# Optimization experiments

Hardware: AMD Instinct MI355X
Metric: run time of the kernel (lower is better)

The kernel has to match this reference:

```python
import jax, jax.numpy as jnp
import numpy as np

B, N, E = 8, 20000, 320000
D_IN, D, D_OUT = 1, 64, 1
EPS = 1e-5


def _layer_norm(z, gamma, beta):
    mu = z.mean(-1, keepdims=True)
    var = ((z - mu) ** 2).mean(-1, keepdims=True)
    return gamma * (z - mu) / jnp.sqrt(var + EPS) + beta


def _mp_layer(h, src, dst, Ws, Wm, bias, gamma, beta):
    # h: (B, N, D); src/dst: (E,)
    h_self = h @ Ws                          # (B, N, D)
    msg = h[:, src, :] @ Wm                  # (B, E, D) gather + GEMM
    h_agg = jnp.zeros_like(h).at[:, dst, :].add(msg)   # scatter-add over nodes
    deg = jnp.zeros((N,), h.dtype).at[dst].add(1.0)
    deg = jnp.maximum(deg, 1.0)
    h_agg = h_agg / deg[None, :, None]
    z = h + jax.nn.relu(h_self + h_agg + bias)  # dropout = identity (eval)
    return _layer_norm(z, gamma, beta)


def setup_inputs() -> dict:
    key = jax.random.key(0)
    ks = jax.random.split(key, 16)
    # weights stored (in, out); y = x @ W + b. Kaiming-normal-ish scale.
    def kaiming(k, fin, fout):
        return jax.random.normal(k, (fin, fout), jnp.float32) * np.sqrt(2.0 / fin)
    inp = {
        "x": jax.random.normal(ks[0], (B, N, D_IN), jnp.float32),
        "edge_index": jax.random.randint(ks[1], (2, E), 0, N),
        "W_in": kaiming(ks[2], D_IN, D), "b_in": jnp.zeros((D,), jnp.float32),
        "Ws1": kaiming(ks[3], D, D), "Wm1": kaiming(ks[4], D, D),
        "bias1": jnp.zeros((D,), jnp.float32),
        "g1": jnp.ones((D,), jnp.float32), "be1": jnp.zeros((D,), jnp.float32),
        "Ws2": kaiming(ks[5], D, D), "Wm2": kaiming(ks[6], D, D),
        "bias2": jnp.zeros((D,), jnp.float32),
        "g2": jnp.ones((D,), jnp.float32), "be2": jnp.zeros((D,), jnp.float32),
        "Wh1": kaiming(ks[7], 2 * D, D), "bh1": jnp.zeros((D,), jnp.float32),
        "Wh2": kaiming(ks[8], D, D_OUT), "bh2": jnp.zeros((D_OUT,), jnp.float32),
    }
    return inp


def reference(x, edge_index, W_in, b_in, Ws1, Wm1, bias1, g1, be1,
              Ws2, Wm2, bias2, g2, be2, Wh1, bh1, Wh2, bh2):
    src, dst = edge_index[0], edge_index[1]
    h = jax.nn.relu(x @ W_in + b_in)                       # (B, N, D)
    h = _mp_layer(h, src, dst, Ws1, Wm1, bias1, g1, be1)
    h = _mp_layer(h, src, dst, Ws2, Wm2, bias2, g2, be2)
    graph_emb = jnp.concatenate([h.mean(axis=1), h.max(axis=1)], axis=-1)  # (B, 2D)
    out = jax.nn.relu(graph_emb @ Wh1 + bh1) @ Wh2 + bh2   # (B, D_OUT)
    return out
```

## Files before the change

### kernel.cpp

```cpp
#include <hip/hip_runtime.h>

#define BB 8
#define NN 20000
#define EE 320000
#define DD 64
#define ROWS (BB*NN)
#define TILES (ROWS/16)
#define EPS 1e-5f
#define CH 64


typedef __attribute__((ext_vector_type(4))) float float4v;
typedef __attribute__((ext_vector_type(8))) _Float16 half8v;

__device__ __forceinline__ int bcasti(int v, int l) {
  return __builtin_amdgcn_readlane(v, l);
}

__global__ __launch_bounds__(256) void k_encoder(const float* __restrict__ x,
    const float* __restrict__ Win, const float* __restrict__ bin,
    _Float16* __restrict__ hH, int* __restrict__ cnt) {
  int idx = blockIdx.x * 256 + threadIdx.x;
  if (idx < NN) cnt[idx] = 0;
  int g = idx * 8;
  if (g < NN * 512) {
    int n = g >> 9;
    int b = (g >> 6) & 7;
    int d0 = g & 63;
    float xv = x[(size_t)b * NN + n];
    float4 w0 = *(const float4*)&Win[d0];
    float4 w1 = *(const float4*)&Win[d0 + 4];
    float4 b0 = *(const float4*)&bin[d0];
    float4 b1 = *(const float4*)&bin[d0 + 4];
    float o[8];
    o[0] = fmaf(xv, w0.x, b0.x); o[1] = fmaf(xv, w0.y, b0.y);
    o[2] = fmaf(xv, w0.z, b0.z); o[3] = fmaf(xv, w0.w, b0.w);
    o[4] = fmaf(xv, w1.x, b1.x); o[5] = fmaf(xv, w1.y, b1.y);
    o[6] = fmaf(xv, w1.z, b1.z); o[7] = fmaf(xv, w1.w, b1.w);
    half8v ho;
#pragma unroll
    for (int k = 0; k < 8; ++k) ho[k] = (_Float16)(o[k] > 0.f ? o[k] : 0.f);
    *(half8v*)&hH[g] = ho;
  }
}

__global__ __launch_bounds__(256) void k_deg(const int* __restrict__ dst,
                                             int* __restrict__ cnt) {
  int e = blockIdx.x * 256 + threadIdx.x;
  if (e < EE) atomicAdd(&cnt[dst[e]], 1);
}

__global__ __launch_bounds__(1024) void k_scan(const int* __restrict__ cnt,
                                               int* __restrict__ rowptr,
                                               int* __restrict__ cur) {
  __shared__ int part[1024];
  int t = threadIdx.x;
  const int PER = (NN + 1023) / 1024;
  int base = t * PER;
  int s = 0;
#pragma unroll
  for (int i = 0; i < PER; ++i) {
    int idx = base + i;
    s += (idx < NN) ? cnt[idx] : 0;
  }
  part[t] = s;
  __syncthreads();
  for (int off = 1; off < 1024; off <<= 1) {
    int v = (t >= off) ? part[t - off] : 0;
    __syncthreads();
    part[t] += v;
    __syncthreads();
  }
  int run = (t > 0) ? part[t - 1] : 0;
#pragma unroll
  for (int i = 0; i < PER; ++i) {
    int idx = base + i;
    if (idx <= NN) rowptr[idx] = run;
    if (idx < NN) cur[idx] = run;
    run += (idx < NN) ? cnt[idx] : 0;
  }
}

__global__ __launch_bounds__(256) void k_fill(const int* __restrict__ src,
    const int* __restrict__ dst, int* __restrict__ cur,
    int* __restrict__ nbr) {
  int e = blockIdx.x * 256 + threadIdx.x;
  if (e < EE) {
    int pos = atomicAdd(&cur[dst[e]], 1);
    nbr[pos] = src[e];
  }
}

__global__ __launch_bounds__(256) void k_agg(const _Float16* __restrict__ hH,
    const int* __restrict__ rowptr, const int* __restrict__ nbr,
    _Float16* __restrict__ aggH) {
  int wid = (blockIdx.x * 256 + threadIdx.x) >> 6;
  int lane = threadIdx.x & 63;
  if (wid >= NN) return;
  int n = wid;
  int s0 = rowptr[n], s1 = rowptr[n + 1];
  float acc[8];
#pragma unroll
  for (int k = 0; k < 8; ++k) acc[k] = 0.f;
  for (int base = s0; base < s1; base += 64) {
    int m = s1 - base;
    if (m > 64) m = 64;
    int idxv = (base + lane < s1) ? nbr[base + lane] : 0;
    int j = 0;
    for (; j + 8 <= m; j += 8) {
      half8v v[8];
#pragma unroll
      for (int i = 0; i < 8; ++i) {
        int s = bcasti(idxv, j + i);
        v[i] = *(const half8v*)(hH + (size_t)s * 512 + lane * 8);
      }
#pragma unroll
      for (int k = 0; k < 8; ++k) {
        float t0 = (float)v[0][k] + (float)v[1][k];
        float t1 = (float)v[2][k] + (float)v[3][k];
        float t2 = (float)v[4][k] + (float)v[5][k];
        float t3 = (float)v[6][k] + (float)v[7][k];
        acc[k] += (t0 + t1) + (t2 + t3);
      }
    }
    for (; j + 4 <= m; j += 4) {
      half8v v[4];
#pragma unroll
      for (int i = 0; i < 4; ++i) {
        int s = bcasti(idxv, j + i);
        v[i] = *(const half8v*)(hH + (size_t)s * 512 + lane * 8);
      }
#pragma unroll
      for (int k = 0; k < 8; ++k) {
        acc[k] += ((float)v[0][k] + (float)v[1][k]) +
                  ((float)v[2][k] + (float)v[3][k]);
      }
    }
    for (; j < m; ++j) {
      int s = bcasti(idxv, j);
      half8v v = *(const half8v*)(hH + (size_t)s * 512 + lane * 8);
#pragma unroll
      for (int k = 0; k < 8; ++k) acc[k] += (float)v[k];
    }
  }
  int deg = s1 - s0;
  float iv = 1.0f / (float)(deg > 1 ? deg : 1);
  half8v o;
#pragma unroll
  for (int k = 0; k < 8; ++k) o[k] = (_Float16)(acc[k] * iv);
  *(half8v*)(aggH + (size_t)n * 512 + lane * 8) = o;
}

__global__ __launch_bounds__(256) void k_node_mfma(
    const _Float16* __restrict__ hH, const _Float16* __restrict__ aggH,
    const float* __restrict__ Ws, const float* __restrict__ Wm,
    const float* __restrict__ bias, const float* __restrict__ g,
    const float* __restrict__ be, _Float16* __restrict__ outH,
    int nwaves_total) {
  __shared__ _Float16 ldsw[16384];
  int tid = threadIdx.x;
  int lane = tid & 63;
  int cidx = lane & 15;
  int grp = lane >> 4;

  for (int m = 0; m < 2; ++m) {
    const float* W = m ? Wm : Ws;
    for (int slot = tid; slot < 512; slot += 256) {
      int c = slot >> 8;
      int t = (slot >> 6) & 3;
      int l = slot & 63;
      int k0 = c * 32 + (l >> 4) * 8;
      int col = t * 16 + (l & 15);
      half8v ohi, olo;
#pragma unroll
      for (int i = 0; i < 8; ++i) {
        float w = W[(k0 + i) * DD + col];
        _Float16 hi = (_Float16)w;
        ohi[i] = hi;
        olo[i] = (_Float16)(w - (float)hi);
      }
      *(half8v*)&ldsw[(((m * 2 + 0) * 2 + c) * 4 + t) * 512 + l * 8] = ohi;
      *(half8v*)&ldsw[(((m * 2 + 1) * 2 + c) * 4 + t) * 512 + l * 8] = olo;
    }
  }
  __syncthreads();

  float bias_c[4], gam_c[4], bet_c[4];
#pragma unroll
  for (int t = 0; t < 4; ++t) {
    int c = t * 16 + cidx;
    bias_c[t] = bias[c];
    gam_c[t] = g[c];
    bet_c[t] = be[c];
  }

  int gwave = blockIdx.x * 4 + (tid >> 6);
  for (int tile = gwave; tile < TILES; tile += nwaves_total) {
    int r0 = tile * 16;
    const _Float16* hp = hH + (size_t)(r0 + cidx) * DD;
    const _Float16* ap = aggH + (size_t)(r0 + cidx) * DD;
    half8v ah[2], am[2];
    ah[0] = *(const half8v*)(hp + grp * 8);
    ah[1] = *(const half8v*)(hp + 32 + grp * 8);
    am[0] = *(const half8v*)(ap + grp * 8);
    am[1] = *(const half8v*)(ap + 32 + grp * 8);

    float4v acc[4];
#pragma unroll
    for (int t = 0; t < 4; ++t) acc[t] = (float4v){0.f, 0.f, 0.f, 0.f};
#pragma unroll
    for (int t = 0; t < 4; ++t) {
#pragma unroll
      for (int c = 0; c < 2; ++c) {
        const half8v bsh = *(const half8v*)&ldsw[((0 + c) * 4 + t) * 512 + lane * 8];
        const half8v bsl = *(const half8v*)&ldsw[((2 + c) * 4 + t) * 512 + lane * 8];
        const half8v bmh = *(const half8v*)&ldsw[((4 + c) * 4 + t) * 512 + lane * 8];
        const half8v bml = *(const half8v*)&ldsw[((6 + c) * 4 + t) * 512 + lane * 8];
        acc[t] = __builtin_amdgcn_mfma_f32_16x16x32_f16(ah[c], bsh, acc[t], 0, 0, 0);
        acc[t] = __builtin_amdgcn_mfma_f32_16x16x32_f16(ah[c], bsl, acc[t], 0, 0, 0);
        acc[t] = __builtin_amdgcn_mfma_f32_16x16x32_f16(am[c], bmh, acc[t], 0, 0, 0);
        acc[t] = __builtin_amdgcn_mfma_f32_16x16x32_f16(am[c], bml, acc[t], 0, 0, 0);
      }
    }
#pragma unroll
    for (int j = 0; j < 4; ++j) {
      int row = r0 + grp * 4 + j;
      const _Float16* hr = hH + (size_t)row * DD;
      float zz[4];
      float part = 0.f;
#pragma unroll
      for (int t = 0; t < 4; ++t) {
        float hv = (float)hr[t * 16 + cidx];
        float v = acc[t][j] + bias_c[t];
        v = v > 0.f ? v : 0.f;
        zz[t] = hv + v;
        part += zz[t];
      }
      part += __shfl_xor(part, 1);
      part += __shfl_xor(part, 2);
      part += __shfl_xor(part, 4);
      part += __shfl_xor(part, 8);
      float mu = part * (1.0f / 64.0f);
      float vs = 0.f;
#pragma unroll
      for (int t = 0; t < 4; ++t) {
        float d = zz[t] - mu;
        vs += d * d;
      }
      vs += __shfl_xor(vs, 1);
      vs += __shfl_xor(vs, 2);
      vs += __shfl_xor(vs, 4);
      vs += __shfl_xor(vs, 8);
      float inv = rsqrtf(vs * (1.0f / 64.0f) + EPS);
#pragma unroll
      for (int t = 0; t < 4; ++t) {
        float val = fmaf(gam_c[t] * (zz[t] - mu), inv, bet_c[t]);
        outH[(size_t)row * DD + t * 16 + cidx] = (_Float16)val;
      }
    }
  }
}

__global__ __launch_bounds__(256) void k_reduce(const _Float16* __restrict__ hH,
    float* __restrict__ psum, float* __restrict__ pmax) {
  int lane = threadIdx.x & 63;
  int w = threadIdx.x >> 6;
  int b = blockIdx.x / CH;
  int chunk = blockIdx.x % CH;
  const int csz = (NN + CH - 1) / CH;
  int n0 = chunk * csz;
  int n1 = n0 + csz;
  if (n1 > NN) n1 = NN;
  float s = 0.f, m = -INFINITY;
  for (int n = n0 + w; n < n1; n += 4) {
    float v = (float)hH[(size_t)n * 512 + b * 64 + lane];
    s += v;
    m = fmaxf(m, v);
  }
  __shared__ float ls[4][DD], lm[4][DD];
  ls[w][lane] = s;
  lm[w][lane] = m;
  __syncthreads();
  if (w == 0) {
    float ss = ls[0][lane] + ls[1][lane] + ls[2][lane] + ls[3][lane];
    float mm = fmaxf(fmaxf(lm[0][lane], lm[1][lane]),
                     fmaxf(lm[2][lane], lm[3][lane]));
    psum[((size_t)b * CH + chunk) * DD + lane] = ss;
    pmax[((size_t)b * CH + chunk) * DD + lane] = mm;
  }
}

__global__ __launch_bounds__(512) void k_final(const float* __restrict__ psum,
    const float* __restrict__ pmax, const float* __restrict__ Wh1,
    const float* __restrict__ bh1, const float* __restrict__ Wh2,
    const float* __restrict__ bh2, float* __restrict__ out) {
  __shared__ float emb[BB][2 * DD];
  __shared__ float hid[BB][DD];
  int t = threadIdx.x;
  int b = t >> 6, d = t & 63;
  float s = 0.f, m = -INFINITY;
  for (int c = 0; c < CH; ++c) {
    s += psum[((size_t)b * CH + c) * DD + d];
    m = fmaxf(m, pmax[((size_t)b * CH + c) * DD + d]);
  }
  emb[b][d] = s * (1.0f / (float)NN);
  emb[b][DD + d] = m;
  __syncthreads();
  float acc = bh1[d];
#pragma unroll
  for (int k = 0; k < 2 * DD; ++k) acc = fmaf(emb[b][k], Wh1[k * DD + d], acc);
  hid[b][d] = acc > 0.f ? acc : 0.f;
  __syncthreads();
  if (d == 0) {
    float o = bh2[0];
    for (int j = 0; j < DD; ++j) o = fmaf(hid[b][j], Wh2[j], o);
    out[b] = o;
  }
}

extern "C" void kernel_launch(void* const* d_in, const int* in_sizes, int n_in,
                              void* d_out, int out_size, void* d_ws, size_t ws_size,
                              hipStream_t stream) {
  const float* x    = (const float*)d_in[0];
  const int*   ei   = (const int*)d_in[1];
  const float* Win  = (const float*)d_in[2];
  const float* bin  = (const float*)d_in[3];
  const float* Ws1  = (const float*)d_in[4];
  const float* Wm1  = (const float*)d_in[5];
  const float* bias1= (const float*)d_in[6];
  const float* g1   = (const float*)d_in[7];
  const float* be1  = (const float*)d_in[8];
  const float* Ws2  = (const float*)d_in[9];
  const float* Wm2  = (const float*)d_in[10];
  const float* bias2= (const float*)d_in[11];
  const float* g2   = (const float*)d_in[12];
  const float* be2  = (const float*)d_in[13];
  const float* Wh1  = (const float*)d_in[14];
  const float* bh1  = (const float*)d_in[15];
  const float* Wh2  = (const float*)d_in[16];
  const float* bh2  = (const float*)d_in[17];
  float* out = (float*)d_out;

  const int* src = ei;
  const int* dst = ei + EE;

  char* ws = (char*)d_ws;
  size_t off = 0;
  auto carve = [&](size_t bytes) {
    void* p = ws + off;
    off = (off + bytes + 255) & ~(size_t)255;
    return p;
  };
  const size_t h16bytes = sizeof(_Float16) * (size_t)ROWS * DD;
  _Float16* hA     = (_Float16*)carve(h16bytes);
  _Float16* hB     = (_Float16*)carve(h16bytes);
  _Float16* aggH   = (_Float16*)carve(h16bytes);
  int*      cnt    = (int*)carve(sizeof(int) * NN);
  int*      cur    = (int*)carve(sizeof(int) * NN);
  int*      rowptr = (int*)carve(sizeof(int) * (NN + 1));
  int*      nbr    = (int*)carve(sizeof(int) * EE);
  float*    psum   = (float*)carve(sizeof(float) * (size_t)BB * CH * DD);
  float*    pmax   = (float*)carve(sizeof(float) * (size_t)BB * CH * DD);

  const int NODE_BLOCKS = 2048;
  const int NODE_WAVES = NODE_BLOCKS * 4;

  k_encoder<<<(NN * 512 / 8 + 255) / 256, 256, 0, stream>>>(x, Win, bin, hA, cnt);

  k_deg<<<(EE + 255) / 256, 256, 0, stream>>>(dst, cnt);
  k_scan<<<1, 1024, 0, stream>>>(cnt, rowptr, cur);
  k_fill<<<(EE + 255) / 256, 256, 0, stream>>>(src, dst, cur, nbr);

  k_agg<<<(NN + 3) / 4, 256, 0, stream>>>(hA, rowptr, nbr, aggH);
  k_node_mfma<<<NODE_BLOCKS, 256, 0, stream>>>(hA, aggH, Ws1, Wm1, bias1, g1,
                                               be1, hB, NODE_WAVES);

  k_agg<<<(NN + 3) / 4, 256, 0, stream>>>(hB, rowptr, nbr, aggH);
  k_node_mfma<<<NODE_BLOCKS, 256, 0, stream>>>(hB, aggH, Ws2, Wm2, bias2, g2,
                                               be2, hA, NODE_WAVES);

  k_reduce<<<BB * CH, 256, 0, stream>>>(hA, psum, pmax);
  k_final<<<1, 512, 0, stream>>>(psum, pmax, Wh1, bh1, Wh2, bh2, out);
}
```

Baseline: 248.3 us.

## Fuse neighbor aggregation into MFMA node update kernel via LDS staging

Merges the gather/mean aggregation kernel into the node-update MFMA kernel. Each wave aggregates two nodes (16 rows of the node-major layout), stages the result in LDS and feeds it straight to the MFMA, so the aggH buffer is never written to or read back from global memory. Weight hi/lo fp16 splitting moves to a separate prep kernel that runs once, and each block just copies the packed weights into LDS. The cost is more LDS per block, and aggregation load imbalance across waves may now stall the MFMA phase.

New measurement: 380.0 us. 1.53x slower.

```diff
diff --git a/kernel.cpp b/kernel.cpp
--- a/kernel.cpp
+++ b/kernel.cpp
@@ -5,7 +5,7 @@
 #define EE 320000
 #define DD 64
 #define ROWS (BB*NN)
-#define TILES (ROWS/16)
+#define TILES (NN/2)
 #define EPS 1e-5f
 #define CH 64
 
@@ -91,98 +91,49 @@
   }
 }
 
-__global__ __launch_bounds__(256) void k_agg(const _Float16* __restrict__ hH,
-    const int* __restrict__ rowptr, const int* __restrict__ nbr,
-    _Float16* __restrict__ aggH) {
-  int wid = (blockIdx.x * 256 + threadIdx.x) >> 6;
-  int lane = threadIdx.x & 63;
-  if (wid >= NN) return;
-  int n = wid;
-  int s0 = rowptr[n], s1 = rowptr[n + 1];
-  float acc[8];
-#pragma unroll
-  for (int k = 0; k < 8; ++k) acc[k] = 0.f;
-  for (int base = s0; base < s1; base += 64) {
-    int m = s1 - base;
-    if (m > 64) m = 64;
-    int idxv = (base + lane < s1) ? nbr[base + lane] : 0;
-    int j = 0;
-    for (; j + 8 <= m; j += 8) {
-      half8v v[8];
-#pragma unroll
-      for (int i = 0; i < 8; ++i) {
-        int s = bcasti(idxv, j + i);
-        v[i] = *(const half8v*)(hH + (size_t)s * 512 + lane * 8);
-      }
-#pragma unroll
-      for (int k = 0; k < 8; ++k) {
-        float t0 = (float)v[0][k] + (float)v[1][k];
-        float t1 = (float)v[2][k] + (float)v[3][k];
-        float t2 = (float)v[4][k] + (float)v[5][k];
-        float t3 = (float)v[6][k] + (float)v[7][k];
-        acc[k] += (t0 + t1) + (t2 + t3);
-      }
-    }
-    for (; j + 4 <= m; j += 4) {
-      half8v v[4];
-#pragma unroll
-      for (int i = 0; i < 4; ++i) {
-        int s = bcasti(idxv, j + i);
-        v[i] = *(const half8v*)(hH + (size_t)s * 512 + lane * 8);
-      }
-#pragma unroll
-      for (int k = 0; k < 8; ++k) {
-        acc[k] += ((float)v[0][k] + (float)v[1][k]) +
-                  ((float)v[2][k] + (float)v[3][k]);
-      }
-    }
-    for (; j < m; ++j) {
-      int s = bcasti(idxv, j);
-      half8v v = *(const half8v*)(hH + (size_t)s * 512 + lane * 8);
-#pragma unroll
-      for (int k = 0; k < 8; ++k) acc[k] += (float)v[k];
-    }
-  }
-  int deg = s1 - s0;
-  float iv = 1.0f / (float)(deg > 1 ? deg : 1);
-  half8v o;
-#pragma unroll
-  for (int k = 0; k < 8; ++k) o[k] = (_Float16)(acc[k] * iv);
-  *(half8v*)(aggH + (size_t)n * 512 + lane * 8) = o;
-}
-
-__global__ __launch_bounds__(256) void k_node_mfma(
-    const _Float16* __restrict__ hH, const _Float16* __restrict__ aggH,
-    const float* __restrict__ Ws, const float* __restrict__ Wm,
+__global__ __launch_bounds__(256) void k_prep(const float* __restrict__ Ws1,
+    const float* __restrict__ Wm1, const float* __restrict__ Ws2,
+    const float* __restrict__ Wm2, _Float16* __restrict__ o1,
+    _Float16* __restrict__ o2) {
+  int gid = blockIdx.x * 256 + threadIdx.x;
+  int layer = gid >> 10;
+  int slot = gid & 1023;
+  int m = slot >> 9;
+  int c = (slot >> 8) & 1;
+  int t = (slot >> 6) & 3;
+  int l = slot & 63;
+  const float* W = layer ? (m ? Wm2 : Ws2) : (m ? Wm1 : Ws1);
+  _Float16* out = layer ? o2 : o1;
+  int k0 = c * 32 + (l >> 4) * 8;
+  int col = t * 16 + (l & 15);
+  half8v ohi, olo;
+#pragma unroll
+  for (int i = 0; i < 8; ++i) {
+    float w = W[(k0 + i) * DD + col];
+    _Float16 hi = (_Float16)w;
+    ohi[i] = hi;
+    olo[i] = (_Float16)(w - (float)hi);
+  }
+  *(half8v*)&out[(((m * 2 + 0) * 2 + c) * 4 + t) * 512 + l * 8] = ohi;
+  *(half8v*)&out[(((m * 2 + 1) * 2 + c) * 4 + t) * 512 + l * 8] = olo;
+}
+
+__global__ __launch_bounds__(256, 4) void k_agg_node(
+    const _Float16* __restrict__ hH, const int* __restrict__ rowptr,
+    const int* __restrict__ nbr, const _Float16* __restrict__ Wsp,
     const float* __restrict__ bias, const float* __restrict__ g,
     const float* __restrict__ be, _Float16* __restrict__ outH,
     int nwaves_total) {
   __shared__ _Float16 ldsw[16384];
+  __shared__ _Float16 ldsa[4][1024];
   int tid = threadIdx.x;
   int lane = tid & 63;
+  int wv = tid >> 6;
   int cidx = lane & 15;
   int grp = lane >> 4;
 
-  for (int m = 0; m < 2; ++m) {
-    const float* W = m ? Wm : Ws;
-    for (int slot = tid; slot < 512; slot += 256) {
-      int c = slot >> 8;
-      int t = (slot >> 6) & 3;
-      int l = slot & 63;
-      int k0 = c * 32 + (l >> 4) * 8;
-      int col = t * 16 + (l & 15);
-      half8v ohi, olo;
-#pragma unroll
-      for (int i = 0; i < 8; ++i) {
-        float w = W[(k0 + i) * DD + col];
-        _Float16 hi = (_Float16)w;
-        ohi[i] = hi;
-        olo[i] = (_Float16)(w - (float)hi);
-      }
-      *(half8v*)&ldsw[(((m * 2 + 0) * 2 + c) * 4 + t) * 512 + l * 8] = ohi;
-      *(half8v*)&ldsw[(((m * 2 + 1) * 2 + c) * 4 + t) * 512 + l * 8] = olo;
-    }
-  }
+  for (int i = tid; i < 2048; i += 256)
+    *(half8v*)&ldsw[i * 8] = *(const half8v*)&Wsp[i * 8];
   __syncthreads();
 
   float bias_c[4], gam_c[4], bet_c[4];
@@ -194,16 +145,71 @@
     bet_c[t] = be[c];
   }
 
-  int gwave = blockIdx.x * 4 + (tid >> 6);
+  int gwave = blockIdx.x * 4 + wv;
   for (int tile = gwave; tile < TILES; tile += nwaves_total) {
+#pragma unroll
+    for (int nn = 0; nn < 2; ++nn) {
+      int n = tile * 2 + nn;
+      int s0 = rowptr[n], s1 = rowptr[n + 1];
+      float acc[8];
+#pragma unroll
+      for (int k = 0; k < 8; ++k) acc[k] = 0.f;
+      for (int base = s0; base < s1; base += 64) {
+        int m = s1 - base;
+        if (m > 64) m = 64;
+        int idxv = (base + lane < s1) ? nbr[base + lane] : 0;
+        int j = 0;
+        for (; j + 8 <= m; j += 8) {
+          half8v v[8];
+#pragma unroll
+          for (int i = 0; i < 8; ++i) {
+            int s = bcasti(idxv, j + i);
+            v[i] = *(const half8v*)(hH + (size_t)s * 512 + lane * 8);
+          }
+#pragma unroll
+          for (int k = 0; k < 8; ++k) {
+            float t0 = (float)v[0][k] + (float)v[1][k];
+            float t1 = (float)v[2][k] + (float)v[3][k];
+            float t2 = (float)v[4][k] + (float)v[5][k];
+            float t3 = (float)v[6][k] + (float)v[7][k];
+            acc[k] += (t0 + t1) + (t2 + t3);
+          }
+        }
+        for (; j + 4 <= m; j += 4) {
+          half8v v[4];
+#pragma unroll
+          for (int i = 0; i < 4; ++i) {
+            int s = bcasti(idxv, j + i);
+            v[i] = *(const half8v*)(hH + (size_t)s * 512 + lane * 8);
+          }
+#pragma unroll
+          for (int k = 0; k < 8; ++k) {
+            acc[k] += ((float)v[0][k] + (float)v[1][k]) +
+                      ((float)v[2][k] + (float)v[3][k]);
+          }
+        }
+        for (; j < m; ++j) {
+          int s = bcasti(idxv, j);
+          half8v v = *(const half8v*)(hH + (size_t)s * 512 + lane * 8);
+#pragma unroll
+          for (int k = 0; k < 8; ++k) acc[k] += (float)v[k];
+        }
+      }
+      int deg = s1 - s0;
+      float iv = 1.0f / (float)(deg > 1 ? deg : 1);
+      half8v o;
+#pragma unroll
+      for (int k = 0; k < 8; ++k) o[k] = (_Float16)(acc[k] * iv);
+      int row = nn * 8 + (lane >> 3);
+      *(half8v*)&ldsa[wv][row * 64 + (lane & 7) * 8] = o;
+    }
+    half8v am[2], ah[2];
+    am[0] = *(const half8v*)&ldsa[wv][cidx * 64 + grp * 8];
+    am[1] = *(const half8v*)&ldsa[wv][cidx * 64 + 32 + grp * 8];
     int r0 = tile * 16;
     const _Float16* hp = hH + (size_t)(r0 + cidx) * DD;
-    const _Float16* ap = aggH + (size_t)(r0 + cidx) * DD;
-    half8v ah[2], am[2];
     ah[0] = *(const half8v*)(hp + grp * 8);
     ah[1] = *(const half8v*)(hp + 32 + grp * 8);
-    am[0] = *(const half8v*)(ap + grp * 8);
-    am[1] = *(const half8v*)(ap + 32 + grp * 8);
 
     float4v acc[4];
 #pragma unroll
@@ -354,7 +360,8 @@
   const size_t h16bytes = sizeof(_Float16) * (size_t)ROWS * DD;
   _Float16* hA     = (_Float16*)carve(h16bytes);
   _Float16* hB     = (_Float16*)carve(h16bytes);
-  _Float16* aggH   = (_Float16*)carve(h16bytes);
+  _Float16* Wsp1   = (_Float16*)carve(sizeof(_Float16) * 16384);
+  _Float16* Wsp2   = (_Float16*)carve(sizeof(_Float16) * 16384);
   int*      cnt    = (int*)carve(sizeof(int) * NN);
   int*      cur    = (int*)carve(sizeof(int) * NN);
   int*      rowptr = (int*)carve(sizeof(int) * (NN + 1));
@@ -362,22 +369,20 @@
   float*    psum   = (float*)carve(sizeof(float) * (size_t)BB * CH * DD);
   float*    pmax   = (float*)carve(sizeof(float) * (size_t)BB * CH * DD);
 
-  const int NODE_BLOCKS = 2048;
+  const int NODE_BLOCKS = 2500;
   const int NODE_WAVES = NODE_BLOCKS * 4;
 
+  k_prep<<<8, 256, 0, stream>>>(Ws1, Wm1, Ws2, Wm2, Wsp1, Wsp2);
   k_encoder<<<(NN * 512 / 8 + 255) / 256, 256, 0, stream>>>(x, Win, bin, hA, cnt);
 
   k_deg<<<(EE + 255) / 256, 256, 0, stream>>>(dst, cnt);
   k_scan<<<1, 1024, 0, stream>>>(cnt, rowptr, cur);
   k_fill<<<(EE + 255) / 256, 256, 0, stream>>>(src, dst, cur, nbr);
 
-  k_agg<<<(NN + 3) / 4, 256, 0, stream>>>(hA, rowptr, nbr, aggH);
-  k_node_mfma<<<NODE_BLOCKS, 256, 0, stream>>>(hA, aggH, Ws1, Wm1, bias1, g1,
-                                               be1, hB, NODE_WAVES);
-
-  k_agg<<<(NN + 3) / 4, 256, 0, stream>>>(hB, rowptr, nbr, aggH);
-  k_node_mfma<<<NODE_BLOCKS, 256, 0, stream>>>(hB, aggH, Ws2, Wm2, bias2, g2,
-                                               be2, hA, NODE_WAVES);
+  k_agg_node<<<NODE_BLOCKS, 256, 0, stream>>>(hA, rowptr, nbr, Wsp1, bias1,
+                                              g1, be1, hB, NODE_WAVES);
+  k_agg_node<<<NODE_BLOCKS, 256, 0, stream>>>(hB, rowptr, nbr, Wsp2, bias2,
+                                              g2, be2, hA, NODE_WAVES);
 
   k_reduce<<<BB * CH, 256, 0, stream>>>(hA, psum, pmax);
   k_final<<<1, 512, 0, stream>>>(psum, pmax, Wh1, bh1, Wh2, bh2, out);
```
